# Performance work log

Measured on AMD Instinct MI355X. Metric: run time of the kernel, lower is better.

## Reference

```python
import jax, jax.numpy as jnp
import numpy as np

S, D, H, MLP = 2048, 1024, 16, 4096
DK = D // H
EPS = 1e-5  # torch LayerNorm default


def setup_inputs() -> dict:
    key = jax.random.key(0)
    ks = jax.random.split(key, 8)
    init = lambda k, shape, fan_in: jax.random.normal(k, shape, jnp.float32) * (fan_in ** -0.5)
    return {
        "x": jax.random.normal(ks[0], (S, D), jnp.float32),
        "wq": init(ks[1], (D, D), D), "bq": jnp.zeros((D,), jnp.float32),
        "wk": init(ks[2], (D, D), D), "bk": jnp.zeros((D,), jnp.float32),
        "wv": init(ks[3], (D, D), D), "bv": jnp.zeros((D,), jnp.float32),
        "wo": init(ks[4], (D, D), D), "bo": jnp.zeros((D,), jnp.float32),
        "w1": init(ks[5], (D, MLP), D), "b1": jnp.zeros((MLP,), jnp.float32),
        "w2": init(ks[6], (MLP, D), MLP), "b2": jnp.zeros((D,), jnp.float32),
        "ln1_g": jnp.ones((D,), jnp.float32), "ln1_b": jnp.zeros((D,), jnp.float32),
        "ln2_g": jnp.ones((D,), jnp.float32), "ln2_b": jnp.zeros((D,), jnp.float32),
    }


def _layernorm(x, g, b):
    m = jnp.mean(x, axis=-1, keepdims=True)
    v = jnp.var(x, axis=-1, keepdims=True)
    return (x - m) * jax.lax.rsqrt(v + EPS) * g + b


def reference(x, wq, bq, wk, bk, wv, bv, wo, bo, w1, b1, w2, b2, ln1_g, ln1_b, ln2_g, ln2_b):
    # --- residual 1: pre-LN multi-head self-attention ---
    h = _layernorm(x, ln1_g, ln1_b)
    q = (h @ wq + bq).reshape(S, H, DK).transpose(1, 0, 2)  # [H,S,DK]
    k = (h @ wk + bk).reshape(S, H, DK).transpose(1, 0, 2)
    v = (h @ wv + bv).reshape(S, H, DK).transpose(1, 0, 2)
    scores = jnp.einsum('hqd,hkd->hqk', q, k) / jnp.sqrt(jnp.float32(DK))  # [H,S,S]
    attn = jax.nn.softmax(scores, axis=-1)
    o = jnp.einsum('hqk,hkd->hqd', attn, v)  # [H,S,DK]
    # Faithful to original: x.contiguous().view(S, -1) is a raw reshape of the
    # [H,S,DK] buffer (no transpose back to [S,H,DK]).
    o = o.reshape(S, D)
    x = x + (o @ wo + bo)
    # --- residual 2: pre-LN GELU FFN ---
    h2 = _layernorm(x, ln2_g, ln2_b)
    f = jax.nn.gelu(h2 @ w1 + b1, approximate=False)  # torch nn.GELU = exact erf
    x = x + (f @ w2 + b2)
    return x
```

## Files before the change

kernel.cpp:

```cpp
#include <hip/hip_runtime.h>


constexpr int kS = 2048, kD = 1024, kH = 16, kDK = 64, kMLP = 4096;
constexpr float kEps = 1e-5f;

using u16 = unsigned short;
using u32 = unsigned int;
typedef float f32x4 __attribute__((ext_vector_type(4)));
typedef short bf16x8 __attribute__((ext_vector_type(8)));

__device__ __forceinline__ u16 f2b(float f) {
  u32 u = __builtin_bit_cast(u32, f);
  return (u16)((u + 0x7fffu + ((u >> 16) & 1u)) >> 16);
}

typedef const __attribute__((address_space(1))) u32* gas1;
typedef __attribute__((address_space(3))) u32* las3;
__device__ __forceinline__ void async16(const void* g, void* l) {
  __builtin_amdgcn_global_load_lds((gas1)g, (las3)l, 16, 0, 0);
}

__global__ __launch_bounds__(256)
void ln_kernel(const float* __restrict__ x, const float* __restrict__ g,
               const float* __restrict__ b, u16* __restrict__ out) {
  __shared__ float red[8];
  const int row = blockIdx.x, tid = threadIdx.x;
  const float4 v = *(const float4*)(x + (size_t)row * kD + tid * 4);
  float s = v.x + v.y + v.z + v.w;
  float ss = v.x * v.x + v.y * v.y + v.z * v.z + v.w * v.w;
#pragma unroll
  for (int d = 1; d < 64; d <<= 1) { s += __shfl_xor(s, d); ss += __shfl_xor(ss, d); }
  if ((tid & 63) == 0) { red[tid >> 6] = s; red[4 + (tid >> 6)] = ss; }
  __syncthreads();
  const float m = (red[0] + red[1] + red[2] + red[3]) * (1.f / kD);
  const float var = (red[4] + red[5] + red[6] + red[7]) * (1.f / kD) - m * m;
  const float r = rsqrtf(var + kEps);
  const float4 gv = *(const float4*)(g + tid * 4);
  const float4 bv = *(const float4*)(b + tid * 4);
  ushort4 o;
  o.x = f2b((v.x - m) * r * gv.x + bv.x);
  o.y = f2b((v.y - m) * r * gv.y + bv.y);
  o.z = f2b((v.z - m) * r * gv.z + bv.z);
  o.w = f2b((v.w - m) * r * gv.w + bv.w);
  *(ushort4*)(out + (size_t)row * kD + tid * 4) = o;
}

__global__ __launch_bounds__(256)
void transpose_cvt(const float* __restrict__ in, u16* __restrict__ out, int R, int C) {
  __shared__ float tile[32][33];
  const int c0 = blockIdx.x * 32, r0 = blockIdx.y * 32;
  const int x = threadIdx.x, y = threadIdx.y;
#pragma unroll
  for (int i = 0; i < 4; ++i)
    tile[y + i * 8][x] = in[(size_t)(r0 + y + i * 8) * C + c0 + x];
  __syncthreads();
#pragma unroll
  for (int i = 0; i < 4; ++i)
    out[(size_t)(c0 + y + i * 8) * R + r0 + x] = f2b(tile[x][y + i * 8]);
}

__global__ void concat_bias(const float* __restrict__ bq, const float* __restrict__ bk,
                            const float* __restrict__ bv, float* __restrict__ out) {
  int i = blockIdx.x * 256 + threadIdx.x;
  out[i] = i < kD ? bq[i] : (i < 2 * kD ? bk[i - kD] : bv[i - 2 * kD]);
}

__global__ __launch_bounds__(256)
void vtrans(const u16* __restrict__ qkv, u16* __restrict__ vt) {
  __shared__ u16 t[64][72];
  const int s0 = blockIdx.x * 64, h = blockIdx.y, tid = threadIdx.x;
#pragma unroll
  for (int r = 0; r < 2; ++r) {
    int chunk = r * 256 + tid, row = chunk >> 3, col = (chunk & 7) * 8;
    uint4 v = *(const uint4*)(qkv + (size_t)(s0 + row) * 3072 + 2 * kD + h * 64 + col);
    *(uint4*)(&t[row][col]) = v;
  }
  __syncthreads();
#pragma unroll
  for (int r = 0; r < 2; ++r) {
    int chunk = r * 256 + tid, drow = chunk >> 3, scol = (chunk & 7) * 8;
    u16 tmp[8];
#pragma unroll
    for (int j = 0; j < 8; ++j) tmp[j] = t[scol + j][drow];
    *(uint4*)(vt + (size_t)h * 64 * kS + (size_t)drow * kS + s0 + scol) = *(uint4*)tmp;
  }
}

template <int BN, int WM, int WN, int EPI>
__global__ __launch_bounds__(256, 2)
void gemm_bt(const u16* __restrict__ A, const u16* __restrict__ Bt,
             const float* __restrict__ bias, const float* __restrict__ res,
             void* __restrict__ Cout, int N, int K) {
  constexpr int BM = 128, BK = 32;
  constexpr int MT = BM / (WM * 16);
  constexpr int NT = BN / (WN * 16);
  constexpr int RA = BM * BK / 2048;
  constexpr int RB = BN * BK / 2048;
  __shared__ u16 As[BM * BK];
  __shared__ u16 Bs[BN * BK];
  const int tid = threadIdx.x;
  const int w = tid >> 6, l = tid & 63;
  const int wm = w / WN, wn = w % WN;
  const int row0 = blockIdx.y * BM, col0 = blockIdx.x * BN;

  const u16* Ag = A + (size_t)(row0 + w * 16 + (l >> 2)) * K + (l & 3) * 8;
  const u16* Bg = Bt + (size_t)(col0 + w * 16 + (l >> 2)) * K + (l & 3) * 8;
  u16* AsW = As + w * 512;
  u16* BsW = Bs + w * 512;

  f32x4 acc[MT][NT] = {};

  for (int kt = 0; kt < K; kt += BK) {
#pragma unroll
    for (int r = 0; r < RA; ++r) async16(Ag + (size_t)r * 64 * K + kt, AsW + r * 2048);
#pragma unroll
    for (int r = 0; r < RB; ++r) async16(Bg + (size_t)r * 64 * K + kt, BsW + r * 2048);
    __syncthreads();
    bf16x8 af[MT], bfr[NT];
#pragma unroll
    for (int i = 0; i < MT; ++i)
      af[i] = *(const bf16x8*)(As + (wm * (BM / WM) + i * 16 + (l & 15)) * BK + (l >> 4) * 8);
#pragma unroll
    for (int j = 0; j < NT; ++j)
      bfr[j] = *(const bf16x8*)(Bs + (wn * (BN / WN) + j * 16 + (l & 15)) * BK + (l >> 4) * 8);
#pragma unroll
    for (int i = 0; i < MT; ++i)
#pragma unroll
      for (int j = 0; j < NT; ++j)
        acc[i][j] = __builtin_amdgcn_mfma_f32_16x16x32_bf16(af[i], bfr[j], acc[i][j], 0, 0, 0);
    __syncthreads();
  }

#pragma unroll
  for (int i = 0; i < MT; ++i) {
    const int row = row0 + wm * (BM / WM) + i * 16 + ((l >> 4) << 2);
#pragma unroll
    for (int j = 0; j < NT; ++j) {
      const int col = col0 + wn * (BN / WN) + j * 16 + (l & 15);
      const float bb = bias[col];
#pragma unroll
      for (int r = 0; r < 4; ++r) {
        const size_t idx = (size_t)(row + r) * N + col;
        float v = acc[i][j][r] + bb;
        if constexpr (EPI == 0) {
          ((u16*)Cout)[idx] = f2b(v);
        } else if constexpr (EPI == 1) {
          ((u16*)Cout)[idx] = f2b(0.5f * v * (1.f + erff(v * 0.7071067811865475f)));
        } else {
          ((float*)Cout)[idx] = v + res[idx];
        }
      }
    }
  }
}

__global__ __launch_bounds__(256, 2)
void flash_attn(const u16* __restrict__ qkv, const u16* __restrict__ vt,
                u16* __restrict__ og) {
  constexpr int LQ = 72;
  constexpr int LV = 136;
  __shared__ u16 Qs[64 * LQ];
  __shared__ u16 Ks[128 * LQ];
  __shared__ u16 Vs[64 * LV];
  __shared__ u16 Ps[4][16 * LV];
  const int tid = threadIdx.x, w = tid >> 6, l = tid & 63;
  const int h = blockIdx.y, q0 = blockIdx.x * 64;

#pragma unroll
  for (int r = 0; r < 2; ++r) {
    int chunk = r * 256 + tid, row = chunk >> 3, col = (chunk & 7) * 8;
    uint4 v = *(const uint4*)(qkv + (size_t)(q0 + row) * 3072 + h * 64 + col);
    *(uint4*)(&Qs[row * LQ + col]) = v;
  }
  __syncthreads();
  bf16x8 qa[2];
#pragma unroll
  for (int kq = 0; kq < 2; ++kq)
    qa[kq] = *(const bf16x8*)(&Qs[(w * 16 + (l & 15)) * LQ + kq * 32 + (l >> 4) * 8]);

  f32x4 oacc[4] = {};
  float mi[4], li[4];
#pragma unroll
  for (int r = 0; r < 4; ++r) { mi[r] = -1e30f; li[r] = 0.f; }

  for (int kt = 0; kt < kS; kt += 128) {
    __syncthreads();
#pragma unroll
    for (int r = 0; r < 4; ++r) {
      int chunk = r * 256 + tid, row = chunk >> 3, col = (chunk & 7) * 8;
      uint4 v = *(const uint4*)(qkv + (size_t)(kt + row) * 3072 + kD + h * 64 + col);
      *(uint4*)(&Ks[row * LQ + col]) = v;
    }
#pragma unroll
    for (int r = 0; r < 4; ++r) {
      int chunk = r * 256 + tid, row = chunk >> 4, col = (chunk & 15) * 8;
      uint4 v = *(const uint4*)(vt + (size_t)h * 64 * kS + (size_t)row * kS + kt + col);
      *(uint4*)(&Vs[row * LV + col]) = v;
    }
    __syncthreads();

    f32x4 s[8];
#pragma unroll
    for (int n = 0; n < 8; ++n) {
      f32x4 z = {};
      bf16x8 kb0 = *(const bf16x8*)(&Ks[(n * 16 + (l & 15)) * LQ + (l >> 4) * 8]);
      bf16x8 kb1 = *(const bf16x8*)(&Ks[(n * 16 + (l & 15)) * LQ + 32 + (l >> 4) * 8]);
      z = __builtin_amdgcn_mfma_f32_16x16x32_bf16(qa[0], kb0, z, 0, 0, 0);
      z = __builtin_amdgcn_mfma_f32_16x16x32_bf16(qa[1], kb1, z, 0, 0, 0);
      s[n] = z;
    }
    float alpha[4];
#pragma unroll
    for (int r = 0; r < 4; ++r) {
      float m = -1e30f;
#pragma unroll
      for (int n = 0; n < 8; ++n) m = fmaxf(m, s[n][r]);
#pragma unroll
      for (int d = 1; d < 16; d <<= 1) m = fmaxf(m, __shfl_xor(m, d));
      m *= 0.125f;
      float mn = fmaxf(mi[r], m);
      alpha[r] = __expf(mi[r] - mn);
      mi[r] = mn;
      li[r] *= alpha[r];
    }
#pragma unroll
    for (int n = 0; n < 4; ++n)
#pragma unroll
      for (int r = 0; r < 4; ++r) oacc[n][r] *= alpha[r];
    float rs[4] = {0.f, 0.f, 0.f, 0.f};
#pragma unroll
    for (int n = 0; n < 8; ++n)
#pragma unroll
      for (int r = 0; r < 4; ++r) {
        float pv = __expf(s[n][r] * 0.125f - mi[r]);
        rs[r] += pv;
        Ps[w][((l >> 4) * 4 + r) * LV + n * 16 + (l & 15)] = f2b(pv);
      }
#pragma unroll
    for (int r = 0; r < 4; ++r) {
      float t = rs[r];
#pragma unroll
      for (int d = 1; d < 16; d <<= 1) t += __shfl_xor(t, d);
      li[r] += t;
    }
    bf16x8 pa[4];
#pragma unroll
    for (int ks = 0; ks < 4; ++ks)
      pa[ks] = *(const bf16x8*)(&Ps[w][(l & 15) * LV + ks * 32 + (l >> 4) * 8]);
#pragma unroll
    for (int n = 0; n < 4; ++n)
#pragma unroll
      for (int ks = 0; ks < 4; ++ks) {
        bf16x8 vb = *(const bf16x8*)(&Vs[(n * 16 + (l & 15)) * LV + ks * 32 + (l >> 4) * 8]);
        oacc[n] = __builtin_amdgcn_mfma_f32_16x16x32_bf16(pa[ks], vb, oacc[n], 0, 0, 0);
      }
  }
#pragma unroll
  for (int r = 0; r < 4; ++r) {
    float inv = 1.f / li[r];
    int srow = q0 + w * 16 + (l >> 4) * 4 + r;
#pragma unroll
    for (int n = 0; n < 4; ++n) {
      int d = n * 16 + (l & 15);
      og[(size_t)h * kS * kDK + (size_t)srow * kDK + d] = f2b(oacc[n][r] * inv);
    }
  }
}

extern "C" void kernel_launch(void* const* d_in, const int* in_sizes, int n_in,
                              void* d_out, int out_size, void* d_ws, size_t ws_size,
                              hipStream_t stream) {
  const float* x = (const float*)d_in[0];
  const float* wq = (const float*)d_in[1];
  const float* bq = (const float*)d_in[2];
  const float* wk = (const float*)d_in[3];
  const float* bk = (const float*)d_in[4];
  const float* wv = (const float*)d_in[5];
  const float* bv = (const float*)d_in[6];
  const float* wo = (const float*)d_in[7];
  const float* bo = (const float*)d_in[8];
  const float* w1 = (const float*)d_in[9];
  const float* b1 = (const float*)d_in[10];
  const float* w2 = (const float*)d_in[11];
  const float* b2 = (const float*)d_in[12];
  const float* ln1g = (const float*)d_in[13];
  const float* ln1b = (const float*)d_in[14];
  const float* ln2g = (const float*)d_in[15];
  const float* ln2b = (const float*)d_in[16];
  float* out = (float*)d_out;

  char* p = (char*)d_ws;
  auto alloc = [&](size_t bytes) { void* q = (void*)p; p += (bytes + 255) & ~(size_t)255; return q; };
  u16* h1 = (u16*)alloc((size_t)kS * kD * 2);
  u16* wqkvt = (u16*)alloc((size_t)3 * kD * kD * 2);
  float* bqkv = (float*)alloc((size_t)3 * kD * 4);
  u16* qkv = (u16*)alloc((size_t)kS * 3 * kD * 2);
  u16* vt = (u16*)alloc((size_t)kH * kDK * kS * 2);
  u16* og = (u16*)alloc((size_t)kS * kD * 2);
  u16* wot = (u16*)alloc((size_t)kD * kD * 2);
  float* x2 = (float*)alloc((size_t)kS * kD * 4);
  u16* h2 = (u16*)alloc((size_t)kS * kD * 2);
  u16* w1t = (u16*)alloc((size_t)kD * kMLP * 2);
  u16* fbuf = (u16*)alloc((size_t)kS * kMLP * 2);
  u16* w2t = (u16*)alloc((size_t)kMLP * kD * 2);

  dim3 tb(32, 8);
  transpose_cvt<<<dim3(kD / 32, kD / 32), tb, 0, stream>>>(wq, wqkvt, kD, kD);
  transpose_cvt<<<dim3(kD / 32, kD / 32), tb, 0, stream>>>(wk, wqkvt + kD * kD, kD, kD);
  transpose_cvt<<<dim3(kD / 32, kD / 32), tb, 0, stream>>>(wv, wqkvt + 2 * kD * kD, kD, kD);
  transpose_cvt<<<dim3(kD / 32, kD / 32), tb, 0, stream>>>(wo, wot, kD, kD);
  transpose_cvt<<<dim3(kMLP / 32, kD / 32), tb, 0, stream>>>(w1, w1t, kD, kMLP);
  transpose_cvt<<<dim3(kD / 32, kMLP / 32), tb, 0, stream>>>(w2, w2t, kMLP, kD);
  concat_bias<<<dim3(12), dim3(256), 0, stream>>>(bq, bk, bv, bqkv);

  ln_kernel<<<dim3(kS), dim3(256), 0, stream>>>(x, ln1g, ln1b, h1);
  gemm_bt<128, 2, 2, 0><<<dim3(3 * kD / 128, kS / 128), dim3(256), 0, stream>>>(
      h1, wqkvt, bqkv, nullptr, qkv, 3 * kD, kD);
  vtrans<<<dim3(kS / 64, kH), dim3(256), 0, stream>>>(qkv, vt);
  flash_attn<<<dim3(kS / 64, kH), dim3(256), 0, stream>>>(qkv, vt, og);
  gemm_bt<64, 4, 1, 2><<<dim3(kD / 64, kS / 128), dim3(256), 0, stream>>>(
      og, wot, bo, x, x2, kD, kD);
  ln_kernel<<<dim3(kS), dim3(256), 0, stream>>>(x2, ln2g, ln2b, h2);
  gemm_bt<128, 2, 2, 1><<<dim3(kMLP / 128, kS / 128), dim3(256), 0, stream>>>(
      h2, w1t, b1, nullptr, fbuf, kMLP, kD);
  gemm_bt<64, 4, 1, 2><<<dim3(kD / 64, kS / 128), dim3(256), 0, stream>>>(
      fbuf, w2t, b2, x2, out, kD, kMLP);
}
```

Measured before the change: 352.5 us.

## Swizzle GEMM LDS layout and split-K the N=1024 projections with a reduce kernel

The GEMM kernel is fixed to 128x128 tiles. Its shared-memory layout gets an XOR swizzle on the k-chunk index to cut LDS bank conflicts on fragment reads. The output projection and the FFN down-projection now split K across grid z (2 and 4 ways) and write fp32 partial sums into a workspace region that reuses dead buffers. A new reduce_add kernel sums the partials with bias and residual. This aims at better tile efficiency and occupancy for the narrow-N GEMMs, at the cost of extra partial-sum memory traffic and one more launch per split GEMM.

```diff
diff --git a/kernel.cpp b/kernel.cpp
--- a/kernel.cpp
+++ b/kernel.cpp
@@ -86,43 +86,47 @@
   }
 }
 
-template <int BN, int WM, int WN, int EPI>
+template <int EPI>
 __global__ __launch_bounds__(256, 2)
 void gemm_bt(const u16* __restrict__ A, const u16* __restrict__ Bt,
-             const float* __restrict__ bias, const float* __restrict__ res,
-             void* __restrict__ Cout, int N, int K) {
-  constexpr int BM = 128, BK = 32;
-  constexpr int MT = BM / (WM * 16);
-  constexpr int NT = BN / (WN * 16);
-  constexpr int RA = BM * BK / 2048;
-  constexpr int RB = BN * BK / 2048;
+             const float* __restrict__ bias, void* __restrict__ Cout,
+             int N, int K, int Ksub) {
+  constexpr int BM = 128, BN = 128, BK = 32;
+  constexpr int MT = 4, NT = 4;
   __shared__ u16 As[BM * BK];
   __shared__ u16 Bs[BN * BK];
   const int tid = threadIdx.x;
   const int w = tid >> 6, l = tid & 63;
-  const int wm = w / WN, wn = w % WN;
+  const int wm = w >> 1, wn = w & 1;
   const int row0 = blockIdx.y * BM, col0 = blockIdx.x * BN;
-
-  const u16* Ag = A + (size_t)(row0 + w * 16 + (l >> 2)) * K + (l & 3) * 8;
-  const u16* Bg = Bt + (size_t)(col0 + w * 16 + (l >> 2)) * K + (l & 3) * 8;
+  const int koff = blockIdx.z * Ksub;
+
+  const int sc = ((l & 3) ^ ((l >> 3) & 3)) * 8;
+  const u16* Ag = A + (size_t)(row0 + w * 16 + (l >> 2)) * K + koff + sc;
+  const u16* Bg = Bt + (size_t)(col0 + w * 16 + (l >> 2)) * K + koff + sc;
   u16* AsW = As + w * 512;
   u16* BsW = Bs + w * 512;
 
   f32x4 acc[MT][NT] = {};
-
-  for (int kt = 0; kt < K; kt += BK) {
-#pragma unroll
-    for (int r = 0; r < RA; ++r) async16(Ag + (size_t)r * 64 * K + kt, AsW + r * 2048);
-#pragma unroll
-    for (int r = 0; r < RB; ++r) async16(Bg + (size_t)r * 64 * K + kt, BsW + r * 2048);
+  const int q = l >> 4;
+
+  for (int kt = 0; kt < Ksub; kt += BK) {
+#pragma unroll
+    for (int r = 0; r < 2; ++r) async16(Ag + (size_t)r * 64 * K + kt, AsW + r * 2048);
+#pragma unroll
+    for (int r = 0; r < 2; ++r) async16(Bg + (size_t)r * 64 * K + kt, BsW + r * 2048);
     __syncthreads();
     bf16x8 af[MT], bfr[NT];
 #pragma unroll
-    for (int i = 0; i < MT; ++i)
-      af[i] = *(const bf16x8*)(As + (wm * (BM / WM) + i * 16 + (l & 15)) * BK + (l >> 4) * 8);
-#pragma unroll
-    for (int j = 0; j < NT; ++j)
-      bfr[j] = *(const bf16x8*)(Bs + (wn * (BN / WN) + j * 16 + (l & 15)) * BK + (l >> 4) * 8);
+    for (int i = 0; i < MT; ++i) {
+      const int ra = wm * 64 + i * 16 + (l & 15);
+      af[i] = *(const bf16x8*)(As + ra * 32 + (q ^ ((ra >> 1) & 3)) * 8);
+    }
+#pragma unroll
+    for (int j = 0; j < NT; ++j) {
+      const int rb = wn * 64 + j * 16 + (l & 15);
+      bfr[j] = *(const bf16x8*)(Bs + rb * 32 + (q ^ ((rb >> 1) & 3)) * 8);
+    }
 #pragma unroll
     for (int i = 0; i < MT; ++i)
 #pragma unroll
@@ -131,13 +135,17 @@
     __syncthreads();
   }
 
+  float* Pf = nullptr;
+  if constexpr (EPI == 3)
+    Pf = (float*)Cout + (size_t)blockIdx.z * gridDim.y * BM * N;
 #pragma unroll
   for (int i = 0; i < MT; ++i) {
-    const int row = row0 + wm * (BM / WM) + i * 16 + ((l >> 4) << 2);
+    const int row = row0 + wm * 64 + i * 16 + ((l >> 4) << 2);
 #pragma unroll
     for (int j = 0; j < NT; ++j) {
-      const int col = col0 + wn * (BN / WN) + j * 16 + (l & 15);
-      const float bb = bias[col];
+      const int col = col0 + wn * 64 + j * 16 + (l & 15);
+      float bb = 0.f;
+      if constexpr (EPI != 3) bb = bias[col];
 #pragma unroll
       for (int r = 0; r < 4; ++r) {
         const size_t idx = (size_t)(row + r) * N + col;
@@ -147,11 +155,28 @@
         } else if constexpr (EPI == 1) {
           ((u16*)Cout)[idx] = f2b(0.5f * v * (1.f + erff(v * 0.7071067811865475f)));
         } else {
-          ((float*)Cout)[idx] = v + res[idx];
+          Pf[idx] = v;
         }
       }
     }
   }
+}
+
+template <int KS>
+__global__ __launch_bounds__(256)
+void reduce_add(const float* __restrict__ parts, const float* __restrict__ bias,
+                const float* __restrict__ res, float* __restrict__ out,
+                int N, size_t strideMN) {
+  const size_t b = ((size_t)blockIdx.x * 256 + threadIdx.x) * 4;
+  float4 a = *(const float4*)(res + b);
+  const float4 bv = *(const float4*)(bias + (b & (size_t)(N - 1)));
+  a.x += bv.x; a.y += bv.y; a.z += bv.z; a.w += bv.w;
+#pragma unroll
+  for (int s = 0; s < KS; ++s) {
+    const float4 p = *(const float4*)(parts + s * strideMN + b);
+    a.x += p.x; a.y += p.y; a.z += p.z; a.w += p.w;
+  }
+  *(float4*)(out + b) = a;
 }
 
 __global__ __launch_bounds__(256, 2)
@@ -293,16 +318,18 @@
   auto alloc = [&](size_t bytes) { void* q = (void*)p; p += (bytes + 255) & ~(size_t)255; return q; };
   u16* h1 = (u16*)alloc((size_t)kS * kD * 2);
   u16* wqkvt = (u16*)alloc((size_t)3 * kD * kD * 2);
-  float* bqkv = (float*)alloc((size_t)3 * kD * 4);
   u16* qkv = (u16*)alloc((size_t)kS * 3 * kD * 2);
   u16* vt = (u16*)alloc((size_t)kH * kDK * kS * 2);
   u16* og = (u16*)alloc((size_t)kS * kD * 2);
   u16* wot = (u16*)alloc((size_t)kD * kD * 2);
-  float* x2 = (float*)alloc((size_t)kS * kD * 4);
   u16* h2 = (u16*)alloc((size_t)kS * kD * 2);
   u16* w1t = (u16*)alloc((size_t)kD * kMLP * 2);
+  float* bqkv = (float*)alloc((size_t)3 * kD * 4);
+  float* x2 = (float*)alloc((size_t)kS * kD * 4);
   u16* fbuf = (u16*)alloc((size_t)kS * kMLP * 2);
   u16* w2t = (u16*)alloc((size_t)kMLP * kD * 2);
+  float* part = (float*)d_ws;
+  const size_t strideMN = (size_t)kS * kD;
 
   dim3 tb(32, 8);
   transpose_cvt<<<dim3(kD / 32, kD / 32), tb, 0, stream>>>(wq, wqkvt, kD, kD);
@@ -314,15 +341,19 @@
   concat_bias<<<dim3(12), dim3(256), 0, stream>>>(bq, bk, bv, bqkv);
 
   ln_kernel<<<dim3(kS), dim3(256), 0, stream>>>(x, ln1g, ln1b, h1);
-  gemm_bt<128, 2, 2, 0><<<dim3(3 * kD / 128, kS / 128), dim3(256), 0, stream>>>(
-      h1, wqkvt, bqkv, nullptr, qkv, 3 * kD, kD);
+  gemm_bt<0><<<dim3(3 * kD / 128, kS / 128, 1), dim3(256), 0, stream>>>(
+      h1, wqkvt, bqkv, qkv, 3 * kD, kD, kD);
   vtrans<<<dim3(kS / 64, kH), dim3(256), 0, stream>>>(qkv, vt);
   flash_attn<<<dim3(kS / 64, kH), dim3(256), 0, stream>>>(qkv, vt, og);
-  gemm_bt<64, 4, 1, 2><<<dim3(kD / 64, kS / 128), dim3(256), 0, stream>>>(
-      og, wot, bo, x, x2, kD, kD);
+  gemm_bt<3><<<dim3(kD / 128, kS / 128, 2), dim3(256), 0, stream>>>(
+      og, wot, nullptr, part, kD, kD, kD / 2);
+  reduce_add<2><<<dim3(kS * kD / 4 / 256), dim3(256), 0, stream>>>(
+      part, bo, x, x2, kD, strideMN);
   ln_kernel<<<dim3(kS), dim3(256), 0, stream>>>(x2, ln2g, ln2b, h2);
-  gemm_bt<128, 2, 2, 1><<<dim3(kMLP / 128, kS / 128), dim3(256), 0, stream>>>(
-      h2, w1t, b1, nullptr, fbuf, kMLP, kD);
-  gemm_bt<64, 4, 1, 2><<<dim3(kD / 64, kS / 128), dim3(256), 0, stream>>>(
-      fbuf, w2t, b2, x2, out, kD, kMLP);
-}
+  gemm_bt<1><<<dim3(kMLP / 128, kS / 128, 1), dim3(256), 0, stream>>>(
+      h2, w1t, b1, fbuf, kMLP, kD, kD);
+  gemm_bt<3><<<dim3(kD / 128, kS / 128, 4), dim3(256), 0, stream>>>(
+      fbuf, w2t, nullptr, part, kD, kMLP, kMLP / 4);
+  reduce_add<4><<<dim3(kS * kD / 4 / 256), dim3(256), 0, stream>>>(
+      part, b2, x2, out, kD, strideMN);
+}
```

Result: faster. 321.5 us (-8.8%).
